# Optimization experiments

Hardware: AMD Instinct MI355X
Metric: run time of the kernel (lower is better)

The kernel has to match this reference:

```python
import jax, jax.numpy as jnp
import numpy as np

DIM = 1024
DEPTH = 4
HEADS = 16
DIM_HEAD = 64
MLP = 4096
INNER = HEADS * DIM_HEAD  # == DIM, so to_out projection present
SCALE = DIM_HEAD ** -0.5
EPS = 1e-5


def layernorm(x, g, b):
    mu = jnp.mean(x, axis=-1, keepdims=True)
    var = jnp.var(x, axis=-1, keepdims=True)
    return (x - mu) * jax.lax.rsqrt(var + EPS) * g + b


def setup_inputs() -> dict:
    key = jax.random.key(0)
    ks = jax.random.split(key, 12)
    B, N = 4, 1024
    s = lambda fan: 1.0 / np.sqrt(fan)
    inp = {
        "x": jax.random.normal(ks[0], (B, N, DIM), jnp.float32),
        "Wqkv": jax.random.normal(ks[1], (DEPTH, DIM, 3 * INNER), jnp.float32) * s(DIM),
        "Wout": jax.random.normal(ks[2], (DEPTH, INNER, DIM), jnp.float32) * s(INNER),
        "bout": jnp.zeros((DEPTH, DIM), jnp.float32),
        "ln1_g": jnp.ones((DEPTH, DIM), jnp.float32),
        "ln1_b": jnp.zeros((DEPTH, DIM), jnp.float32),
        "W1": jax.random.normal(ks[3], (DEPTH, DIM, MLP), jnp.float32) * s(DIM),
        "b1": jnp.zeros((DEPTH, MLP), jnp.float32),
        "W2": jax.random.normal(ks[4], (DEPTH, MLP, DIM), jnp.float32) * s(MLP),
        "b2": jnp.zeros((DEPTH, DIM), jnp.float32),
        "ln2_g": jnp.ones((DEPTH, DIM), jnp.float32),
        "ln2_b": jnp.zeros((DEPTH, DIM), jnp.float32),
        "masks_np": jax.random.randint(ks[5], (B, N), 0, 2, jnp.int32),
        "masks_bert": jax.random.randint(ks[6], (B, N), 0, 2, jnp.int32),
    }
    return inp


def reference(x, Wqkv, Wout, bout, ln1_g, ln1_b, W1, b1, W2, b2, ln2_g, ln2_b,
              masks_np, masks_bert):
    B, N, _ = x.shape
    # pairwise mask: masks_np_[b,i,j] = masks_np[b,i] * masks_np[b,j]
    np_pair = (masks_np[:, :, None] * masks_np[:, None, :])[:, None, :, :]  # [B,1,N,N]
    bert_col = masks_bert[:, None, None, :]                                  # [B,1,1,N]
    for l in range(DEPTH):
        # --- PreNorm masked attention ---
        h = layernorm(x, ln1_g[l], ln1_b[l])
        qkv = h @ Wqkv[l]                                   # [B,N,3*INNER]
        q, k, v = jnp.split(qkv, 3, axis=-1)
        rs = lambda t: t.reshape(B, N, HEADS, DIM_HEAD).transpose(0, 2, 1, 3)
        q, k, v = rs(q), rs(k), rs(v)                       # [B,H,N,D]
        dots = jnp.einsum('bhid,bhjd->bhij', q, k) * SCALE  # [B,H,N,N]
        dots = jnp.where(np_pair == 0, -1000.0, dots)
        dots = jnp.where(bert_col == 1, -1000.0, dots)
        attn = jax.nn.softmax(dots, axis=-1)
        out = jnp.einsum('bhij,bhjd->bhid', attn, v)        # [B,H,N,D]
        out = out.transpose(0, 2, 1, 3).reshape(B, N, INNER)
        x = x + (out @ Wout[l] + bout[l])
        # --- PreNorm FFN ---
        h2 = layernorm(x, ln2_g[l], ln2_b[l])
        h2 = jax.nn.gelu(h2 @ W1[l] + b1[l], approximate=False)
        x = x + (h2 @ W2[l] + b2[l])
    return x
```

## Files before the change

kernel.cpp:

```cpp
#include <hip/hip_runtime.h>
#include <hip/hip_bf16.h>

#define DEPTH 4
#define HEADS 16
#define DIMH  64
#define DIM   1024
#define MLPD  4096
#define NTOK  1024
#define BATCH 4
#define ROWS  (BATCH*NTOK)
#define SCALE 0.125f

typedef float f32x4 __attribute__((ext_vector_type(4)));
typedef short s16x8 __attribute__((ext_vector_type(8)));

#define MFMA(a,b,c) __builtin_amdgcn_mfma_f32_16x16x32_bf16((a),(b),(c),0,0,0)

__device__ __forceinline__ unsigned short f2bf(float f){
  union{ __hip_bfloat16 h; unsigned short u; } x; x.h = __float2bfloat16(f); return x.u;
}
__device__ __forceinline__ float bf2f(unsigned short u){
  return __uint_as_float(((unsigned)u)<<16);
}

__device__ __forceinline__ void async16(const void* g, void* l){
  __builtin_amdgcn_global_load_lds(
      (const __attribute__((address_space(1))) void*)g,
      (__attribute__((address_space(3))) void*)l, 16, 0, 0);
}

__global__ __launch_bounds__(256) void wt_kernel(const float* __restrict__ src,
    unsigned short* __restrict__ dst, int K, int N)
{
  __shared__ float t[64][65];
  int n0 = blockIdx.x*64, k0 = blockIdx.y*64;
  src += (size_t)blockIdx.z*K*N;
  dst += (size_t)blockIdx.z*N*K;
  int tid = threadIdx.x;
  int r = tid>>4, c4 = (tid&15)*4;
#pragma unroll
  for (int p=0;p<4;p++){
    int row = r + p*16;
    float4 v = *(const float4*)(src + (size_t)(k0+row)*N + n0 + c4);
    t[c4+0][row]=v.x; t[c4+1][row]=v.y; t[c4+2][row]=v.z; t[c4+3][row]=v.w;
  }
  __syncthreads();
  int rn = tid>>2, ch = tid&3;
  unsigned short o[16];
#pragma unroll
  for (int i=0;i<16;i++) o[i] = f2bf(t[rn][ch*16+i]);
  uint4* d = (uint4*)(dst + (size_t)(n0+rn)*K + k0 + ch*16);
  d[0] = ((uint4*)o)[0]; d[1] = ((uint4*)o)[1];
}

__global__ __launch_bounds__(256) void ln_kernel(const float* __restrict__ x,
    const float* __restrict__ g, const float* __restrict__ b,
    unsigned short* __restrict__ h)
{
  int row  = blockIdx.x*4 + (threadIdx.x>>6);
  int lane = threadIdx.x & 63;
  const float* xr = x + (size_t)row*DIM;
  float4 v[4]; float s=0.f, ss=0.f;
#pragma unroll
  for (int c=0;c<4;c++){
    v[c] = *(const float4*)(xr + c*256 + lane*4);
    s  += v[c].x+v[c].y+v[c].z+v[c].w;
    ss += v[c].x*v[c].x+v[c].y*v[c].y+v[c].z*v[c].z+v[c].w*v[c].w;
  }
#pragma unroll
  for (int o=1;o<64;o<<=1){ s += __shfl_xor(s,o); ss += __shfl_xor(ss,o); }
  float mu  = s*(1.f/1024.f);
  float var = ss*(1.f/1024.f) - mu*mu;
  float rstd = rsqrtf(var + 1e-5f);
#pragma unroll
  for (int c=0;c<4;c++){
    float4 gg = *(const float4*)(g + c*256 + lane*4);
    float4 bb = *(const float4*)(b + c*256 + lane*4);
    ushort4 o;
    o.x = f2bf((v[c].x-mu)*rstd*gg.x + bb.x);
    o.y = f2bf((v[c].y-mu)*rstd*gg.y + bb.y);
    o.z = f2bf((v[c].z-mu)*rstd*gg.z + bb.z);
    o.w = f2bf((v[c].w-mu)*rstd*gg.w + bb.w);
    *(ushort4*)(h + (size_t)row*DIM + c*256 + lane*4) = o;
  }
}

__global__ __launch_bounds__(256) void vtrans_kernel(
    const unsigned short* __restrict__ qkv, unsigned short* __restrict__ vT)
{
  __shared__ float t[64][65];
  int n0 = blockIdx.x*64;
  int bh = blockIdx.y; int b = bh>>4, hh = bh&15;
  int tid = threadIdx.x;
  int r = tid>>4, c4 = (tid&15)*4;
#pragma unroll
  for (int p=0;p<4;p++){
    int row = r + p*16;
    ushort4 u = *(const ushort4*)(qkv + (size_t)(b*NTOK + n0 + row)*3072 + 2048 + hh*64 + c4);
    t[c4+0][row]=bf2f(u.x); t[c4+1][row]=bf2f(u.y); t[c4+2][row]=bf2f(u.z); t[c4+3][row]=bf2f(u.w);
  }
  __syncthreads();
  int rn = tid>>2, ch = tid&3;
  unsigned short o[16];
#pragma unroll
  for (int i=0;i<16;i++) o[i] = f2bf(t[rn][ch*16+i]);
  uint4* d = (uint4*)(vT + (size_t)(bh*64 + rn)*NTOK + n0 + ch*16);
  d[0] = ((uint4*)o)[0]; d[1] = ((uint4*)o)[1];
}

template<int BN, int EPI>
__global__ __launch_bounds__(256) void gemm_kernel(
    const unsigned short* __restrict__ A,
    const unsigned short* __restrict__ Bt,
    unsigned short* __restrict__ outb,
    float* __restrict__ outf,
    const float* __restrict__ res,
    const float* __restrict__ bias,
    int M, int N, int K, int ldout)
{
  constexpr int BM=128, BK=64;
  constexpr int NT = BN/32;
  __shared__ unsigned short As[BM*BK];
  __shared__ unsigned short Bs[BN*BK];
  int tid = threadIdx.x, lane = tid&63, w = tid>>6;
  int wm = w&1, wn = w>>1;

  int gn  = N/BN;
  int nwg = (M/BM)*gn;
  int bid = blockIdx.x;
  int id  = (nwg%8==0) ? ((bid&7)*(nwg>>3) + (bid>>3)) : bid;
  int m0 = (id/gn)*BM, n0 = (id%gn)*BN;

  f32x4 acc[4][NT] = {};

  for (int k0=0; k0<K; k0+=BK){
    __syncthreads();
#pragma unroll
    for (int i=0;i<4;i++){
      int off = w*4096 + i*1024 + lane*16;
      int row = off>>7, p = (off&127)>>4;
      async16(A + (size_t)(m0+row)*K + k0 + ((p^(row&7))<<3),
              (char*)As + w*4096 + i*1024);
    }
#pragma unroll
    for (int i=0;i<NT;i++){
      int off = w*(BN*32) + i*1024 + lane*16;
      int row = off>>7, p = (off&127)>>4;
      async16(Bt + (size_t)(n0+row)*K + k0 + ((p^(row&7))<<3),
              (char*)Bs + w*(BN*32) + i*1024);
    }
    __syncthreads();
#pragma unroll
    for (int ks=0;ks<2;ks++){
      s16x8 a[4], bfr[NT];
#pragma unroll
      for (int mt=0;mt<4;mt++){
        int row = wm*64 + mt*16 + (lane&15);
        int c = (ks*4 + (lane>>4)) ^ (row&7);
        a[mt] = *(const s16x8*)((const char*)As + row*128 + c*16);
      }
#pragma unroll
      for (int nt=0;nt<NT;nt++){
        int row = wn*(BN/2) + nt*16 + (lane&15);
        int c = (ks*4 + (lane>>4)) ^ (row&7);
        bfr[nt] = *(const s16x8*)((const char*)Bs + row*128 + c*16);
      }
#pragma unroll
      for (int mt=0;mt<4;mt++)
#pragma unroll
        for (int nt=0;nt<NT;nt++)
          acc[mt][nt] = MFMA(a[mt], bfr[nt], acc[mt][nt]);
    }
  }

#pragma unroll
  for (int mt=0;mt<4;mt++)
#pragma unroll
    for (int nt=0;nt<NT;nt++)
#pragma unroll
      for (int r=0;r<4;r++){
        int row = m0 + wm*64 + mt*16 + ((lane>>4)<<2) + r;
        int col = n0 + wn*(BN/2) + nt*16 + (lane&15);
        float v = acc[mt][nt][r];
        if (EPI==0){
          outb[(size_t)row*ldout + col] = f2bf(v);
        } else if (EPI==1){
          float t = v + res[(size_t)row*ldout + col] + bias[col];
          outf[(size_t)row*ldout + col] = t;
        } else {
          float t = v + bias[col];
          t = 0.5f*t*(1.f + erff(t*0.70710678118f));
          outb[(size_t)row*ldout + col] = f2bf(t);
        }
      }
}

template<int EPI>
__global__ __launch_bounds__(512,2) void gemm256_kernel(
    const unsigned short* __restrict__ A,
    const unsigned short* __restrict__ Bt,
    unsigned short* __restrict__ outb,
    const float* __restrict__ bias,
    int M, int N, int K, int ldout)
{
  __shared__ unsigned short lds[2][2][256*64];
  const int tid = threadIdx.x, lane = tid&63, w = tid>>6;
  const int wm = w>>2, wn = w&3;
  const int gn = N>>8;
  const int nwg = (M>>8)*gn;
  const int q = nwg>>3, r = nwg&7;
  const int xc = blockIdx.x&7, od = blockIdx.x>>3;
  const int id = (xc<r ? xc*(q+1) : r*(q+1)+(xc-r)*q) + od;
  const int m0 = (id/gn)<<8, n0 = (id%gn)<<8;
  const int nkt = K>>6;

  f32x4 acc[8][4] = {};
  s16x8 af[8][2];
  s16x8 bf[2][2];

  auto stage = [&](int bsel, int half, int kt){
    const unsigned short* src = (half<2) ? A : Bt;
    const int base0 = (half<2) ? m0 : n0;
    const int rbase = (half&1)<<7;
    char* dstbase = (char*)lds[bsel][half>>1] + (rbase<<7);
#pragma unroll
    for (int i=0;i<2;i++){
      int off  = ((w<<1)+i)<<10;
      int loff = off + lane*16;
      int row  = loff>>7, p = (loff&127)>>4;
      async16(src + (size_t)(base0+rbase+row)*K + (kt<<6) + ((p^(row&7))<<3),
              dstbase + off);
    }
  };

#define LDA(mt,ks) { int rw=(wm<<7)+((mt)<<4)+(lane&15); int pc=(((ks)<<2)+(lane>>4))^(rw&7); \
  af[mt][ks] = *(const s16x8*)((const char*)lds[cur][0] + rw*128 + (pc<<4)); }
#define LDB(j,nt,ks) { int rw=(wn<<6)+((nt)<<4)+(lane&15); int pc=(((ks)<<2)+(lane>>4))^(rw&7); \
  bf[j][ks] = *(const s16x8*)((const char*)lds[cur][1] + rw*128 + (pc<<4)); }

  stage(0,0,0); stage(0,1,0); stage(0,2,0); stage(0,3,0);
  stage(1,0,1); stage(1,1,1);
  asm volatile("s_waitcnt vmcnt(4)" ::: "memory");
  __builtin_amdgcn_s_barrier();

  for (int t=0; t<nkt; ++t){
    const int cur = t&1, nxt = cur^1;
#pragma unroll
    for (int mt=0;mt<4;mt++){ LDA(mt,0); LDA(mt,1); }
#pragma unroll
    for (int nt=0;nt<2;nt++){ LDB(nt,nt,0); LDB(nt,nt,1); }
    if (t+1<nkt) stage(nxt,2,t+1);
    __builtin_amdgcn_s_barrier();
    asm volatile("s_waitcnt lgkmcnt(0)" ::: "memory");
    __builtin_amdgcn_sched_barrier(0);
    __builtin_amdgcn_s_setprio(1);
#pragma unroll
    for (int mt=0;mt<4;mt++)
#pragma unroll
      for (int nt=0;nt<2;nt++){
        acc[mt][nt] = MFMA(af[mt][0], bf[nt][0], acc[mt][nt]);
        acc[mt][nt] = MFMA(af[mt][1], bf[nt][1], acc[mt][nt]);
      }
    __builtin_amdgcn_s_setprio(0);
    __builtin_amdgcn_s_barrier();
#pragma unroll
    for (int mt=4;mt<8;mt++){ LDA(mt,0); LDA(mt,1); }
    if (t+1<nkt) stage(nxt,3,t+1);
    __builtin_amdgcn_s_barrier();
    asm volatile("s_waitcnt lgkmcnt(0)" ::: "memory");
    __builtin_amdgcn_sched_barrier(0);
    __builtin_amdgcn_s_setprio(1);
#pragma unroll
    for (int mt=4;mt<8;mt++)
#pragma unroll
      for (int nt=0;nt<2;nt++){
        acc[mt][nt] = MFMA(af[mt][0], bf[nt][0], acc[mt][nt]);
        acc[mt][nt] = MFMA(af[mt][1], bf[nt][1], acc[mt][nt]);
      }
    __builtin_amdgcn_s_setprio(0);
    __builtin_amdgcn_s_barrier();
#pragma unroll
    for (int nt=0;nt<2;nt++){ LDB(nt,nt+2,0); LDB(nt,nt+2,1); }
    if (t+2<nkt) stage(cur,0,t+2);
    __builtin_amdgcn_s_barrier();
    asm volatile("s_waitcnt lgkmcnt(0)" ::: "memory");
    __builtin_amdgcn_sched_barrier(0);
    __builtin_amdgcn_s_setprio(1);
#pragma unroll
    for (int mt=0;mt<4;mt++)
#pragma unroll
      for (int nt=0;nt<2;nt++){
        acc[mt][nt+2] = MFMA(af[mt][0], bf[nt][0], acc[mt][nt+2]);
        acc[mt][nt+2] = MFMA(af[mt][1], bf[nt][1], acc[mt][nt+2]);
      }
    __builtin_amdgcn_s_setprio(0);
    __builtin_amdgcn_s_barrier();
    if (t+2<nkt) stage(cur,1,t+2);
    __builtin_amdgcn_s_barrier();
    __builtin_amdgcn_s_setprio(1);
#pragma unroll
    for (int mt=4;mt<8;mt++)
#pragma unroll
      for (int nt=0;nt<2;nt++){
        acc[mt][nt+2] = MFMA(af[mt][0], bf[nt][0], acc[mt][nt+2]);
        acc[mt][nt+2] = MFMA(af[mt][1], bf[nt][1], acc[mt][nt+2]);
      }
    __builtin_amdgcn_s_setprio(0);
    if (t+2<nkt) asm volatile("s_waitcnt vmcnt(4)" ::: "memory");
    else         asm volatile("s_waitcnt vmcnt(0)" ::: "memory");
    __builtin_amdgcn_s_barrier();
  }
#undef LDA
#undef LDB

#pragma unroll
  for (int mt=0;mt<8;mt++)
#pragma unroll
    for (int nt=0;nt<4;nt++)
#pragma unroll
      for (int rr=0;rr<4;rr++){
        int row = m0 + (wm<<7) + (mt<<4) + ((lane>>4)<<2) + rr;
        int col = n0 + (wn<<6) + (nt<<4) + (lane&15);
        float v = acc[mt][nt][rr];
        if (EPI==2){
          v += bias[col];
          v = 0.5f*v*(1.f + erff(v*0.70710678118f));
        }
        outb[(size_t)row*ldout + col] = f2bf(v);
      }
}

__global__ __launch_bounds__(256) void attn_kernel(
    const unsigned short* __restrict__ qkv,
    const unsigned short* __restrict__ vT,
    const int* __restrict__ mnp, const int* __restrict__ mbert,
    unsigned short* __restrict__ outb)
{
  __shared__ unsigned short Ks[2][64*64];
  __shared__ unsigned short Vs[2][64*64];
  __shared__ unsigned short Pb[4][16*64];
  __shared__ float fm[NTOK];
  int qt = blockIdx.x, bh = blockIdx.y;
  int b = bh>>4, hh = bh&15;
  int tid = threadIdx.x, lane = tid&63, w = tid>>6;

  for (int j = tid; j < NTOK; j += 256)
    fm[j] = (mnp[b*NTOK+j]==0 || mbert[b*NTOK+j]==1) ? 1.f : 0.f;

  int iA = qt*64 + w*16 + (lane&15);
  s16x8 aq[2];
#pragma unroll
  for (int ks=0;ks<2;ks++)
    aq[ks] = *(const s16x8*)(qkv + (size_t)(b*NTOK+iA)*3072 + hh*64 + ks*32 + ((lane>>4)<<3));

  bool rowm[4]; float mreg[4], lsum[4]; f32x4 o[4];
#pragma unroll
  for (int r=0;r<4;r++){
    int i = qt*64 + w*16 + ((lane>>4)<<2) + r;
    rowm[r] = (mnp[b*NTOK+i]==0);
    mreg[r] = -1e30f; lsum[r] = 0.f;
    o[r] = f32x4{0.f,0.f,0.f,0.f};
  }
  __syncthreads();

  auto stageKV = [&](int bufi, int kc){
    int j0 = kc<<6;
#pragma unroll
    for (int i=0;i<2;i++){
      int off  = w*2048 + i*1024;
      int loff = off + lane*16;
      int row  = loff>>7, p = (loff&127)>>4;
      async16(qkv + (size_t)(b*NTOK + j0 + row)*3072 + 1024 + hh*64 + ((p^(row&7))<<3),
              (char*)Ks[bufi] + off);
      async16(vT + (size_t)(bh*64 + row)*NTOK + j0 + ((p^(row&7))<<3),
              (char*)Vs[bufi] + off);
    }
  };

  stageKV(0,0);

  for (int kc=0; kc<16; kc++){
    int cur = kc&1;
    int j0 = kc*64;
    if (kc<15) stageKV(cur^1, kc+1);
    if (kc<15) asm volatile("s_waitcnt vmcnt(4)" ::: "memory");
    else       asm volatile("s_waitcnt vmcnt(0)" ::: "memory");
    __builtin_amdgcn_s_barrier();

    f32x4 sc[4];
    __builtin_amdgcn_s_setprio(1);
#pragma unroll
    for (int jt=0;jt<4;jt++){
      sc[jt] = f32x4{0.f,0.f,0.f,0.f};
#pragma unroll
      for (int ks=0;ks<2;ks++){
        int row = jt*16 + (lane&15);
        int c = (ks*4 + (lane>>4)) ^ (row&7);
        s16x8 bk = *(const s16x8*)((const char*)Ks[cur] + row*128 + c*16);
        sc[jt] = MFMA(aq[ks], bk, sc[jt]);
      }
    }
    __builtin_amdgcn_s_setprio(0);
#pragma unroll
    for (int jt=0;jt<4;jt++){
      float f = fm[j0 + jt*16 + (lane&15)];
#pragma unroll
      for (int r=0;r<4;r++){
        float s = sc[jt][r]*SCALE;
        sc[jt][r] = (f!=0.f || rowm[r]) ? -1000.f : s;
      }
    }
#pragma unroll
    for (int r=0;r<4;r++){
      float mx = fmaxf(fmaxf(sc[0][r],sc[1][r]), fmaxf(sc[2][r],sc[3][r]));
#pragma unroll
      for (int ofs=8;ofs>=1;ofs>>=1) mx = fmaxf(mx, __shfl_xor(mx, ofs));
      float mnew  = fmaxf(mreg[r], mx);
      float alpha = __expf(mreg[r]-mnew);
      mreg[r] = mnew;
      float rs = 0.f;
#pragma unroll
      for (int jt=0;jt<4;jt++){ float p = __expf(sc[jt][r]-mnew); sc[jt][r]=p; rs+=p; }
      lsum[r] = lsum[r]*alpha + rs;
#pragma unroll
      for (int nt=0;nt<4;nt++) o[nt][r] *= alpha;
    }
#pragma unroll
    for (int jt=0;jt<4;jt++)
#pragma unroll
      for (int r=0;r<4;r++){
        int ir = ((lane>>4)<<2)+r, jc = jt*16+(lane&15);
        int byteoff = ir*128 + ((((jc>>3))^(ir&7))<<4) + ((jc&7)<<1);
        *((unsigned short*)((char*)Pb[w] + byteoff)) = f2bf(sc[jt][r]);
      }
    __builtin_amdgcn_s_setprio(1);
#pragma unroll
    for (int ks=0;ks<2;ks++){
      int rowp = lane&15;
      int cp = (ks*4 + (lane>>4)) ^ (rowp&7);
      s16x8 ap = *(const s16x8*)((const char*)Pb[w] + rowp*128 + cp*16);
#pragma unroll
      for (int nt=0;nt<4;nt++){
        int d = nt*16 + (lane&15);
        int c = (ks*4 + (lane>>4)) ^ (d&7);
        s16x8 bv = *(const s16x8*)((const char*)Vs[cur] + d*128 + c*16);
        o[nt] = MFMA(ap, bv, o[nt]);
      }
    }
    __builtin_amdgcn_s_setprio(0);
    __builtin_amdgcn_s_barrier();
  }

#pragma unroll
  for (int r=0;r<4;r++){
#pragma unroll
    for (int ofs=8;ofs>=1;ofs>>=1) lsum[r] += __shfl_xor(lsum[r], ofs);
    float inv = 1.f/lsum[r];
    int i = qt*64 + w*16 + ((lane>>4)<<2) + r;
#pragma unroll
    for (int nt=0;nt<4;nt++){
      int d = nt*16 + (lane&15);
      outb[(size_t)(b*NTOK+i)*DIM + hh*64 + d] = f2bf(o[nt][r]*inv);
    }
  }
}

extern "C" void kernel_launch(void* const* d_in, const int* in_sizes, int n_in,
                              void* d_out, int out_size, void* d_ws, size_t ws_size,
                              hipStream_t stream)
{
  const float* xin0 = (const float*)d_in[0];
  const float* Wqkv = (const float*)d_in[1];
  const float* Wout = (const float*)d_in[2];
  const float* bout = (const float*)d_in[3];
  const float* ln1g = (const float*)d_in[4];
  const float* ln1b = (const float*)d_in[5];
  const float* W1   = (const float*)d_in[6];
  const float* b1   = (const float*)d_in[7];
  const float* W2   = (const float*)d_in[8];
  const float* b2   = (const float*)d_in[9];
  const float* ln2g = (const float*)d_in[10];
  const float* ln2b = (const float*)d_in[11];
  const int*   mnp  = (const int*)d_in[12];
  const int*   mbt  = (const int*)d_in[13];
  float* out = (float*)d_out;

  unsigned short* Wqkv_t = (unsigned short*)d_ws;
  unsigned short* Wout_t = Wqkv_t + (size_t)4*3072*1024;
  unsigned short* W1_t   = Wout_t + (size_t)4*1024*1024;
  unsigned short* W2_t   = W1_t   + (size_t)4*4096*1024;
  float*          x      = (float*)(W2_t + (size_t)4*1024*4096);
  unsigned short* hbuf   = (unsigned short*)(x + (size_t)ROWS*DIM);
  unsigned short* qkvb   = hbuf  + (size_t)ROWS*DIM;
  unsigned short* vTb    = qkvb  + (size_t)ROWS*3072;
  unsigned short* attnb  = vTb   + (size_t)ROWS*DIM;
  unsigned short* gbuf   = attnb + (size_t)ROWS*DIM;

  wt_kernel<<<dim3(3072/64,1024/64,4),256,0,stream>>>(Wqkv, Wqkv_t, 1024, 3072);
  wt_kernel<<<dim3(1024/64,1024/64,4),256,0,stream>>>(Wout, Wout_t, 1024, 1024);
  wt_kernel<<<dim3(4096/64,1024/64,4),256,0,stream>>>(W1,   W1_t,   1024, 4096);
  wt_kernel<<<dim3(1024/64,4096/64,4),256,0,stream>>>(W2,   W2_t,   4096, 1024);

  for (int l=0;l<4;l++){
    const float* xres = (l==0) ? xin0 : x;
    ln_kernel<<<1024,256,0,stream>>>(xres, ln1g+l*DIM, ln1b+l*DIM, hbuf);
    gemm256_kernel<0><<<192,512,0,stream>>>(hbuf, Wqkv_t + (size_t)l*3072*1024,
        qkvb, nullptr, ROWS, 3072, 1024, 3072);
    vtrans_kernel<<<dim3(16,64),256,0,stream>>>(qkvb, vTb);
    attn_kernel<<<dim3(16,64),256,0,stream>>>(qkvb, vTb, mnp, mbt, attnb);
    gemm_kernel<64,1><<<512,256,0,stream>>>(attnb, Wout_t + (size_t)l*1024*1024,
        nullptr, x, xres, bout+l*DIM, ROWS, 1024, 1024, 1024);
    ln_kernel<<<1024,256,0,stream>>>(x, ln2g+l*DIM, ln2b+l*DIM, hbuf);
    gemm256_kernel<2><<<256,512,0,stream>>>(hbuf, W1_t + (size_t)l*4096*1024,
        gbuf, b1+l*MLPD, ROWS, 4096, 1024, 4096);
    float* xo = (l==3) ? out : x;
    gemm_kernel<64,1><<<512,256,0,stream>>>(gbuf, W2_t + (size_t)l*1024*4096,
        nullptr, xo, x, b2+l*DIM, ROWS, 1024, 4096, 1024);
  }
}
```

Measured before the change: 1.217 ms.

## Rework GEMM pipeline, split-K the FFN down projection, widen attention query tiles

The 256x256 GEMM now uses a K-step of 32 with a three-slot LDS ring and a simpler single-phase MFMA loop in place of the staged double-buffered loop. The kernel also gains split-K support. The W2 projection uses this with four K slices that write bf16 partials into the reused hbuf/qkv space, and a new elementwise kernel sums the partials with the bias and residual. Attention blocks now handle 128 query rows, so each K/V tile is reused twice, and the running-max rescale is skipped unless the max grows by more than 8. The aims are better K/V reuse, fewer W2 tail effects and less loop overhead. The risks are LDS bank conflicts from the unswizzled 64-byte rows, extra memory traffic for the partials, and bf16 rounding of those partials.

```diff
diff --git a/kernel.cpp b/kernel.cpp
--- a/kernel.cpp
+++ b/kernel.cpp
@@ -196,122 +196,81 @@
 }
 
 template<int EPI>
-__global__ __launch_bounds__(512,2) void gemm256_kernel(
+__global__ __launch_bounds__(512,2) void gemm_tb_kernel(
     const unsigned short* __restrict__ A,
     const unsigned short* __restrict__ Bt,
     unsigned short* __restrict__ outb,
     const float* __restrict__ bias,
-    int M, int N, int K, int ldout)
-{
-  __shared__ unsigned short lds[2][2][256*64];
+    int M, int N, int K, int lda, int ldout, int SK, size_t oslab)
+{
+  __shared__ unsigned short lds[3][2][256*32];
   const int tid = threadIdx.x, lane = tid&63, w = tid>>6;
   const int wm = w>>2, wn = w&3;
   const int gn = N>>8;
-  const int nwg = (M>>8)*gn;
-  const int q = nwg>>3, r = nwg&7;
-  const int xc = blockIdx.x&7, od = blockIdx.x>>3;
-  const int id = (xc<r ? xc*(q+1) : r*(q+1)+(xc-r)*q) + od;
-  const int m0 = (id/gn)<<8, n0 = (id%gn)<<8;
-  const int nkt = K>>6;
+  const int ntile = (M>>8)*gn;
+  const int nwg = ntile*SK;
+  int id;
+  { const int q = nwg>>3, r = nwg&7, xc = blockIdx.x&7, od = blockIdx.x>>3;
+    id = (xc<r ? xc*(q+1) : r*(q+1)+(xc-r)*q) + od; }
+  const int sk = id/ntile, tt = id%ntile;
+  const int m0 = (tt/gn)<<8, n0 = (tt%gn)<<8;
+  const int kbase = sk*K;
+  unsigned short* outp = outb + (size_t)sk*oslab;
+  const int nkt = K>>5;
 
   f32x4 acc[8][4] = {};
-  s16x8 af[8][2];
-  s16x8 bf[2][2];
-
-  auto stage = [&](int bsel, int half, int kt){
-    const unsigned short* src = (half<2) ? A : Bt;
-    const int base0 = (half<2) ? m0 : n0;
-    const int rbase = (half&1)<<7;
-    char* dstbase = (char*)lds[bsel][half>>1] + (rbase<<7);
+
+  auto stage = [&](int bsel, int kt){
+    const int k0 = kbase + (kt<<5);
 #pragma unroll
     for (int i=0;i<2;i++){
       int off  = ((w<<1)+i)<<10;
       int loff = off + lane*16;
-      int row  = loff>>7, p = (loff&127)>>4;
-      async16(src + (size_t)(base0+rbase+row)*K + (kt<<6) + ((p^(row&7))<<3),
-              dstbase + off);
+      int row  = loff>>6, cl = (loff&63)>>4;
+      async16(A + (size_t)(m0+row)*lda + k0 + (cl<<3),
+              (char*)lds[bsel][0] + off);
+    }
+#pragma unroll
+    for (int i=0;i<2;i++){
+      int off  = ((w<<1)+i)<<10;
+      int loff = off + lane*16;
+      int row  = loff>>6, cl = (loff&63)>>4;
+      async16(Bt + (size_t)(n0+row)*lda + k0 + (cl<<3),
+              (char*)lds[bsel][1] + off);
     }
   };
 
-#define LDA(mt,ks) { int rw=(wm<<7)+((mt)<<4)+(lane&15); int pc=(((ks)<<2)+(lane>>4))^(rw&7); \
-  af[mt][ks] = *(const s16x8*)((const char*)lds[cur][0] + rw*128 + (pc<<4)); }
-#define LDB(j,nt,ks) { int rw=(wn<<6)+((nt)<<4)+(lane&15); int pc=(((ks)<<2)+(lane>>4))^(rw&7); \
-  bf[j][ks] = *(const s16x8*)((const char*)lds[cur][1] + rw*128 + (pc<<4)); }
-
-  stage(0,0,0); stage(0,1,0); stage(0,2,0); stage(0,3,0);
-  stage(1,0,1); stage(1,1,1);
+  stage(0,0); stage(1,1);
   asm volatile("s_waitcnt vmcnt(4)" ::: "memory");
   __builtin_amdgcn_s_barrier();
 
+  int cb = 0;
   for (int t=0; t<nkt; ++t){
-    const int cur = t&1, nxt = cur^1;
-#pragma unroll
-    for (int mt=0;mt<4;mt++){ LDA(mt,0); LDA(mt,1); }
-#pragma unroll
-    for (int nt=0;nt<2;nt++){ LDB(nt,nt,0); LDB(nt,nt,1); }
-    if (t+1<nkt) stage(nxt,2,t+1);
-    __builtin_amdgcn_s_barrier();
-    asm volatile("s_waitcnt lgkmcnt(0)" ::: "memory");
-    __builtin_amdgcn_sched_barrier(0);
+    int sb = cb+2; if (sb>=3) sb -= 3;
+    if (t+2<nkt) stage(sb, t+2);
+    s16x8 af[8], bf[4];
+#pragma unroll
+    for (int mt=0;mt<8;mt++){
+      int rw = (wm<<7) + (mt<<4) + (lane&15);
+      af[mt] = *(const s16x8*)((const char*)lds[cb][0] + rw*64 + ((lane>>4)<<4));
+    }
+#pragma unroll
+    for (int nt=0;nt<4;nt++){
+      int rw = (wn<<6) + (nt<<4) + (lane&15);
+      bf[nt] = *(const s16x8*)((const char*)lds[cb][1] + rw*64 + ((lane>>4)<<4));
+    }
     __builtin_amdgcn_s_setprio(1);
 #pragma unroll
-    for (int mt=0;mt<4;mt++)
-#pragma unroll
-      for (int nt=0;nt<2;nt++){
-        acc[mt][nt] = MFMA(af[mt][0], bf[nt][0], acc[mt][nt]);
-        acc[mt][nt] = MFMA(af[mt][1], bf[nt][1], acc[mt][nt]);
-      }
-    __builtin_amdgcn_s_setprio(0);
-    __builtin_amdgcn_s_barrier();
-#pragma unroll
-    for (int mt=4;mt<8;mt++){ LDA(mt,0); LDA(mt,1); }
-    if (t+1<nkt) stage(nxt,3,t+1);
-    __builtin_amdgcn_s_barrier();
-    asm volatile("s_waitcnt lgkmcnt(0)" ::: "memory");
-    __builtin_amdgcn_sched_barrier(0);
-    __builtin_amdgcn_s_setprio(1);
-#pragma unroll
-    for (int mt=4;mt<8;mt++)
-#pragma unroll
-      for (int nt=0;nt<2;nt++){
-        acc[mt][nt] = MFMA(af[mt][0], bf[nt][0], acc[mt][nt]);
-        acc[mt][nt] = MFMA(af[mt][1], bf[nt][1], acc[mt][nt]);
-      }
-    __builtin_amdgcn_s_setprio(0);
-    __builtin_amdgcn_s_barrier();
-#pragma unroll
-    for (int nt=0;nt<2;nt++){ LDB(nt,nt+2,0); LDB(nt,nt+2,1); }
-    if (t+2<nkt) stage(cur,0,t+2);
-    __builtin_amdgcn_s_barrier();
-    asm volatile("s_waitcnt lgkmcnt(0)" ::: "memory");
-    __builtin_amdgcn_sched_barrier(0);
-    __builtin_amdgcn_s_setprio(1);
-#pragma unroll
-    for (int mt=0;mt<4;mt++)
-#pragma unroll
-      for (int nt=0;nt<2;nt++){
-        acc[mt][nt+2] = MFMA(af[mt][0], bf[nt][0], acc[mt][nt+2]);
-        acc[mt][nt+2] = MFMA(af[mt][1], bf[nt][1], acc[mt][nt+2]);
-      }
-    __builtin_amdgcn_s_setprio(0);
-    __builtin_amdgcn_s_barrier();
-    if (t+2<nkt) stage(cur,1,t+2);
-    __builtin_amdgcn_s_barrier();
-    __builtin_amdgcn_s_setprio(1);
-#pragma unroll
-    for (int mt=4;mt<8;mt++)
-#pragma unroll
-      for (int nt=0;nt<2;nt++){
-        acc[mt][nt+2] = MFMA(af[mt][0], bf[nt][0], acc[mt][nt+2]);
-        acc[mt][nt+2] = MFMA(af[mt][1], bf[nt][1], acc[mt][nt+2]);
-      }
+    for (int mt=0;mt<8;mt++)
+#pragma unroll
+      for (int nt=0;nt<4;nt++)
+        acc[mt][nt] = MFMA(af[mt], bf[nt], acc[mt][nt]);
     __builtin_amdgcn_s_setprio(0);
     if (t+2<nkt) asm volatile("s_waitcnt vmcnt(4)" ::: "memory");
     else         asm volatile("s_waitcnt vmcnt(0)" ::: "memory");
     __builtin_amdgcn_s_barrier();
-  }
-#undef LDA
-#undef LDB
+    cb = cb+1; if (cb>=3) cb = 0;
+  }
 
 #pragma unroll
   for (int mt=0;mt<8;mt++)
@@ -326,8 +285,26 @@
           v += bias[col];
           v = 0.5f*v*(1.f + erff(v*0.70710678118f));
         }
-        outb[(size_t)row*ldout + col] = f2bf(v);
-      }
+        outp[(size_t)row*ldout + col] = f2bf(v);
+      }
+}
+
+__global__ __launch_bounds__(256) void mlp2add_kernel(
+    const unsigned short* __restrict__ p, const float* __restrict__ x,
+    const float* __restrict__ b2, float* __restrict__ out)
+{
+  int idx = blockIdx.x*256 + threadIdx.x;
+  int i4 = idx<<2;
+  int col = i4 & (DIM-1);
+  float4 v = *(const float4*)(x + i4);
+  float4 bb = *(const float4*)(b2 + col);
+  v.x+=bb.x; v.y+=bb.y; v.z+=bb.z; v.w+=bb.w;
+#pragma unroll
+  for (int s=0;s<4;s++){
+    ushort4 u = *(const ushort4*)(p + (size_t)s*ROWS*DIM + i4);
+    v.x += bf2f(u.x); v.y += bf2f(u.y); v.z += bf2f(u.z); v.w += bf2f(u.w);
+  }
+  *(float4*)(out + i4) = v;
 }
 
 __global__ __launch_bounds__(256) void attn_kernel(
@@ -338,7 +315,7 @@
 {
   __shared__ unsigned short Ks[2][64*64];
   __shared__ unsigned short Vs[2][64*64];
-  __shared__ unsigned short Pb[4][16*64];
+  __shared__ unsigned short Pb[4][2][16*64];
   __shared__ float fm[NTOK];
   int qt = blockIdx.x, bh = blockIdx.y;
   int b = bh>>4, hh = bh&15;
@@ -347,19 +324,21 @@
   for (int j = tid; j < NTOK; j += 256)
     fm[j] = (mnp[b*NTOK+j]==0 || mbert[b*NTOK+j]==1) ? 1.f : 0.f;
 
-  int iA = qt*64 + w*16 + (lane&15);
-  s16x8 aq[2];
-#pragma unroll
-  for (int ks=0;ks<2;ks++)
-    aq[ks] = *(const s16x8*)(qkv + (size_t)(b*NTOK+iA)*3072 + hh*64 + ks*32 + ((lane>>4)<<3));
-
-  bool rowm[4]; float mreg[4], lsum[4]; f32x4 o[4];
-#pragma unroll
-  for (int r=0;r<4;r++){
-    int i = qt*64 + w*16 + ((lane>>4)<<2) + r;
-    rowm[r] = (mnp[b*NTOK+i]==0);
-    mreg[r] = -1e30f; lsum[r] = 0.f;
-    o[r] = f32x4{0.f,0.f,0.f,0.f};
+  s16x8 aq[2][2];
+  bool rowm[2][4]; float mreg[2][4], lsum[2][4]; f32x4 o[2][4];
+#pragma unroll
+  for (int s=0;s<2;s++){
+    int iA = qt*128 + s*64 + w*16 + (lane&15);
+#pragma unroll
+    for (int ks=0;ks<2;ks++)
+      aq[s][ks] = *(const s16x8*)(qkv + (size_t)(b*NTOK+iA)*3072 + hh*64 + ks*32 + ((lane>>4)<<3));
+#pragma unroll
+    for (int nt=0;nt<4;nt++){
+      int i = qt*128 + s*64 + w*16 + ((lane>>4)<<2) + nt;
+      rowm[s][nt] = (mnp[b*NTOK+i]==0);
+      mreg[s][nt] = -1e30f; lsum[s][nt] = 0.f;
+      o[s][nt] = f32x4{0.f,0.f,0.f,0.f};
+    }
   }
   __syncthreads();
 
@@ -387,64 +366,97 @@
     else       asm volatile("s_waitcnt vmcnt(0)" ::: "memory");
     __builtin_amdgcn_s_barrier();
 
-    f32x4 sc[4];
+    float colf[4];
+#pragma unroll
+    for (int jt=0;jt<4;jt++) colf[jt] = fm[j0 + jt*16 + (lane&15)];
+
+    f32x4 sc[2][4];
     __builtin_amdgcn_s_setprio(1);
 #pragma unroll
     for (int jt=0;jt<4;jt++){
-      sc[jt] = f32x4{0.f,0.f,0.f,0.f};
+      sc[0][jt] = f32x4{0.f,0.f,0.f,0.f};
+      sc[1][jt] = f32x4{0.f,0.f,0.f,0.f};
 #pragma unroll
       for (int ks=0;ks<2;ks++){
         int row = jt*16 + (lane&15);
         int c = (ks*4 + (lane>>4)) ^ (row&7);
         s16x8 bk = *(const s16x8*)((const char*)Ks[cur] + row*128 + c*16);
-        sc[jt] = MFMA(aq[ks], bk, sc[jt]);
+        sc[0][jt] = MFMA(aq[0][ks], bk, sc[0][jt]);
+        sc[1][jt] = MFMA(aq[1][ks], bk, sc[1][jt]);
       }
     }
     __builtin_amdgcn_s_setprio(0);
-#pragma unroll
-    for (int jt=0;jt<4;jt++){
-      float f = fm[j0 + jt*16 + (lane&15)];
+
+#pragma unroll
+    for (int s=0;s<2;s++)
+#pragma unroll
+      for (int jt=0;jt<4;jt++)
+#pragma unroll
+        for (int r=0;r<4;r++){
+          float sv = sc[s][jt][r]*SCALE;
+          sc[s][jt][r] = (colf[jt]!=0.f || rowm[s][r]) ? -1000.f : sv;
+        }
+
+    bool need = false;
+    float pmax[2][4];
+#pragma unroll
+    for (int s=0;s<2;s++)
 #pragma unroll
       for (int r=0;r<4;r++){
-        float s = sc[jt][r]*SCALE;
-        sc[jt][r] = (f!=0.f || rowm[r]) ? -1000.f : s;
-      }
-    }
-#pragma unroll
-    for (int r=0;r<4;r++){
-      float mx = fmaxf(fmaxf(sc[0][r],sc[1][r]), fmaxf(sc[2][r],sc[3][r]));
-#pragma unroll
-      for (int ofs=8;ofs>=1;ofs>>=1) mx = fmaxf(mx, __shfl_xor(mx, ofs));
-      float mnew  = fmaxf(mreg[r], mx);
-      float alpha = __expf(mreg[r]-mnew);
-      mreg[r] = mnew;
-      float rs = 0.f;
-#pragma unroll
-      for (int jt=0;jt<4;jt++){ float p = __expf(sc[jt][r]-mnew); sc[jt][r]=p; rs+=p; }
-      lsum[r] = lsum[r]*alpha + rs;
-#pragma unroll
-      for (int nt=0;nt<4;nt++) o[nt][r] *= alpha;
-    }
-#pragma unroll
-    for (int jt=0;jt<4;jt++)
-#pragma unroll
-      for (int r=0;r<4;r++){
-        int ir = ((lane>>4)<<2)+r, jc = jt*16+(lane&15);
-        int byteoff = ir*128 + ((((jc>>3))^(ir&7))<<4) + ((jc&7)<<1);
-        *((unsigned short*)((char*)Pb[w] + byteoff)) = f2bf(sc[jt][r]);
-      }
+        float mx = fmaxf(fmaxf(sc[s][0][r],sc[s][1][r]), fmaxf(sc[s][2][r],sc[s][3][r]));
+#pragma unroll
+        for (int ofs=8;ofs>=1;ofs>>=1) mx = fmaxf(mx, __shfl_xor(mx, ofs));
+        pmax[s][r] = mx;
+        need = need || (mx - mreg[s][r] > 8.f);
+      }
+    if (__any(need)){
+#pragma unroll
+      for (int s=0;s<2;s++)
+#pragma unroll
+        for (int r=0;r<4;r++){
+          float mnew  = fmaxf(mreg[s][r], pmax[s][r]);
+          float alpha = __expf(mreg[s][r]-mnew);
+          mreg[s][r] = mnew;
+          lsum[s][r] *= alpha;
+#pragma unroll
+          for (int nt=0;nt<4;nt++) o[s][nt][r] *= alpha;
+        }
+    }
+
+#pragma unroll
+    for (int s=0;s<2;s++)
+#pragma unroll
+      for (int jt=0;jt<4;jt++)
+#pragma unroll
+        for (int r=0;r<4;r++){
+          float p = __expf(sc[s][jt][r]-mreg[s][r]);
+          sc[s][jt][r] = p; lsum[s][r] += p;
+        }
+#pragma unroll
+    for (int s=0;s<2;s++)
+#pragma unroll
+      for (int jt=0;jt<4;jt++)
+#pragma unroll
+        for (int r=0;r<4;r++){
+          int ir = ((lane>>4)<<2)+r, jc = jt*16+(lane&15);
+          int byteoff = ir*128 + ((((jc>>3))^(ir&7))<<4) + ((jc&7)<<1);
+          *((unsigned short*)((char*)Pb[w][s] + byteoff)) = f2bf(sc[s][jt][r]);
+        }
+
     __builtin_amdgcn_s_setprio(1);
 #pragma unroll
     for (int ks=0;ks<2;ks++){
       int rowp = lane&15;
       int cp = (ks*4 + (lane>>4)) ^ (rowp&7);
-      s16x8 ap = *(const s16x8*)((const char*)Pb[w] + rowp*128 + cp*16);
+      s16x8 ap0 = *(const s16x8*)((const char*)Pb[w][0] + rowp*128 + cp*16);
+      s16x8 ap1 = *(const s16x8*)((const char*)Pb[w][1] + rowp*128 + cp*16);
 #pragma unroll
       for (int nt=0;nt<4;nt++){
         int d = nt*16 + (lane&15);
         int c = (ks*4 + (lane>>4)) ^ (d&7);
         s16x8 bv = *(const s16x8*)((const char*)Vs[cur] + d*128 + c*16);
-        o[nt] = MFMA(ap, bv, o[nt]);
+        o[0][nt] = MFMA(ap0, bv, o[0][nt]);
+        o[1][nt] = MFMA(ap1, bv, o[1][nt]);
       }
     }
     __builtin_amdgcn_s_setprio(0);
@@ -452,17 +464,20 @@
   }
 
 #pragma unroll
-  for (int r=0;r<4;r++){
-#pragma unroll
-    for (int ofs=8;ofs>=1;ofs>>=1) lsum[r] += __shfl_xor(lsum[r], ofs);
-    float inv = 1.f/lsum[r];
-    int i = qt*64 + w*16 + ((lane>>4)<<2) + r;
-#pragma unroll
-    for (int nt=0;nt<4;nt++){
-      int d = nt*16 + (lane&15);
-      outb[(size_t)(b*NTOK+i)*DIM + hh*64 + d] = f2bf(o[nt][r]*inv);
-    }
-  }
+  for (int s=0;s<2;s++)
+#pragma unroll
+    for (int r=0;r<4;r++){
+      float ls = lsum[s][r];
+#pragma unroll
+      for (int ofs=8;ofs>=1;ofs>>=1) ls += __shfl_xor(ls, ofs);
+      float inv = 1.f/ls;
+      int i = qt*128 + s*64 + w*16 + ((lane>>4)<<2) + r;
+#pragma unroll
+      for (int nt=0;nt<4;nt++){
+        int d = nt*16 + (lane&15);
+        outb[(size_t)(b*NTOK+i)*DIM + hh*64 + d] = f2bf(o[s][nt][r]*inv);
+      }
+    }
 }
 
 extern "C" void kernel_launch(void* const* d_in, const int* in_sizes, int n_in,
@@ -495,6 +510,7 @@
   unsigned short* vTb    = qkvb  + (size_t)ROWS*3072;
   unsigned short* attnb  = vTb   + (size_t)ROWS*DIM;
   unsigned short* gbuf   = attnb + (size_t)ROWS*DIM;
+  unsigned short* pbuf   = hbuf;
 
   wt_kernel<<<dim3(3072/64,1024/64,4),256,0,stream>>>(Wqkv, Wqkv_t, 1024, 3072);
   wt_kernel<<<dim3(1024/64,1024/64,4),256,0,stream>>>(Wout, Wout_t, 1024, 1024);
@@ -504,17 +520,18 @@
   for (int l=0;l<4;l++){
     const float* xres = (l==0) ? xin0 : x;
     ln_kernel<<<1024,256,0,stream>>>(xres, ln1g+l*DIM, ln1b+l*DIM, hbuf);
-    gemm256_kernel<0><<<192,512,0,stream>>>(hbuf, Wqkv_t + (size_t)l*3072*1024,
-        qkvb, nullptr, ROWS, 3072, 1024, 3072);
+    gemm_tb_kernel<0><<<192,512,0,stream>>>(hbuf, Wqkv_t + (size_t)l*3072*1024,
+        qkvb, nullptr, ROWS, 3072, 1024, 1024, 3072, 1, 0);
     vtrans_kernel<<<dim3(16,64),256,0,stream>>>(qkvb, vTb);
-    attn_kernel<<<dim3(16,64),256,0,stream>>>(qkvb, vTb, mnp, mbt, attnb);
+    attn_kernel<<<dim3(8,64),256,0,stream>>>(qkvb, vTb, mnp, mbt, attnb);
     gemm_kernel<64,1><<<512,256,0,stream>>>(attnb, Wout_t + (size_t)l*1024*1024,
         nullptr, x, xres, bout+l*DIM, ROWS, 1024, 1024, 1024);
     ln_kernel<<<1024,256,0,stream>>>(x, ln2g+l*DIM, ln2b+l*DIM, hbuf);
-    gemm256_kernel<2><<<256,512,0,stream>>>(hbuf, W1_t + (size_t)l*4096*1024,
-        gbuf, b1+l*MLPD, ROWS, 4096, 1024, 4096);
+    gemm_tb_kernel<2><<<256,512,0,stream>>>(hbuf, W1_t + (size_t)l*4096*1024,
+        gbuf, b1+l*MLPD, ROWS, 4096, 1024, 1024, 4096, 1, 0);
+    gemm_tb_kernel<0><<<256,512,0,stream>>>(gbuf, W2_t + (size_t)l*1024*4096,
+        pbuf, nullptr, ROWS, 1024, 1024, 4096, 1024, 4, (size_t)ROWS*DIM);
     float* xo = (l==3) ? out : x;
-    gemm_kernel<64,1><<<512,256,0,stream>>>(gbuf, W2_t + (size_t)l*1024*4096,
-        nullptr, xo, x, b2+l*DIM, ROWS, 1024, 4096, 1024);
-  }
-}
+    mlp2add_kernel<<<ROWS*DIM/1024,256,0,stream>>>(pbuf, x, b2+l*DIM, xo);
+  }
+}
```

Result: no change. 1.193 ms (-1.9%).
